# Kernel optimization log

Hardware: AMD Instinct MI355X
Metric: run time of the kernel (lower is better)

## Reference

```python
import jax, jax.numpy as jnp
import numpy as np

N_NODES = 100000
N_EDGES = 1600000
D_NODE = 32
D_EDGE = 16
D_OUT = 32
L2_EPS = 1e-12  # tf.math.l2_normalize default epsilon


def setup_inputs() -> dict:
    key = jax.random.key(0)
    k_h, k_e, k_w, k_s, k_d = jax.random.split(key, 5)
    h = jax.random.normal(k_h, (N_NODES, D_NODE), dtype=jnp.float32)
    e = jax.random.normal(k_e, (N_EDGES, D_EDGE), dtype=jnp.float32)
    # Dense(output_dim) kernel over concat(node, edge) features
    W = jax.random.normal(k_w, (D_NODE + D_EDGE, D_OUT), dtype=jnp.float32) * 0.1
    b = jnp.zeros((D_OUT,), dtype=jnp.float32)
    src = jax.random.randint(k_s, (N_EDGES,), 0, N_NODES, dtype=jnp.int32)
    dst = jax.random.randint(k_d, (N_EDGES,), 0, N_NODES, dtype=jnp.int32)
    return {"h": h, "e": e, "W": W, "b": b, "src": src, "dst": dst}


def reference(h, e, W, b, src, dst):
    # message: m = concat(h[src], e)              [E, D+De]
    # reduce:  new_h = mean over (self_msg, mailbox) of Dense(msg)
    # Dense is affine (activation=None), so Dense(mean) == mean(Dense): one GEMM.
    n = h.shape[0]
    msg = jnp.concatenate([h[src], e], axis=-1)                      # [E, D+De]
    agg = jax.ops.segment_sum(msg, dst, num_segments=n)              # [N, D+De]
    deg = jax.ops.segment_sum(jnp.ones_like(dst, dtype=h.dtype), dst, num_segments=n)
    self_msg = jnp.concatenate([h, jnp.zeros((n, e.shape[1]), h.dtype)], axis=-1)
    mean_msg = (self_msg + agg) / (deg[:, None] + 1.0)               # self counts in the mean
    new_h = mean_msg @ W + b                                         # [N, D_OUT]
    # activation=None -> identity; then tf.math.l2_normalize(axis=-1)
    sq = jnp.sum(new_h * new_h, axis=-1, keepdims=True)
    return new_h * jax.lax.rsqrt(jnp.maximum(sq, L2_EPS))
```

## Files before the change

kernel.cpp:

```cpp
#include <hip/hip_runtime.h>

#define D_NODE 32
#define D_EDGE 16
#define D_IN   48
#define D_OUT  32
#define L2_EPS 1e-12f

#define NPB       128
#define BKT_SHIFT 7
#define MAX_NB    4096
#define CH        8192
#define CTH       1024
#define EPT       (CH / CTH)
#define GR        128
#define TILE      512
#define ATH       512


__global__ __launch_bounds__(CTH) void k_chunkhist(
    const int* __restrict__ dst, int* __restrict__ counts2d, int n_edges, int nb)
{
    extern __shared__ int c[];
    for (int i = threadIdx.x; i < nb; i += CTH) c[i] = 0;
    __syncthreads();
    int base = blockIdx.x * CH + threadIdx.x;
    #pragma unroll
    for (int k = 0; k < EPT; ++k) {
        int i = base + k * CTH;
        if (i < n_edges) atomicAdd(&c[dst[i] >> BKT_SHIFT], 1);
    }
    __syncthreads();
    int* row = counts2d + (size_t)blockIdx.x * nb;
    for (int i = threadIdx.x; i < nb; i += CTH) row[i] = c[i];
}

__global__ __launch_bounds__(256) void k_partial(
    const int* __restrict__ counts2d, int* __restrict__ partial, int nb, int nc)
{
    int b = blockIdx.x * 256 + threadIdx.x;
    if (b >= nb) return;
    int g = blockIdx.y;
    int c0 = g * GR, c1 = min(c0 + GR, nc);
    int s = 0;
    #pragma unroll 4
    for (int c = c0; c < c1; ++c) s += counts2d[(size_t)c * nb + b];
    partial[(size_t)g * nb + b] = s;
}

__global__ __launch_bounds__(1024) void k_offsets(
    int* __restrict__ partial, int* __restrict__ offsets, int nb, int ng)
{
    __shared__ int s[1024];
    const int PT = MAX_NB / 1024;
    int t = threadIdx.x;
    int tot[PT];
    int ts = 0;
    #pragma unroll
    for (int j = 0; j < PT; ++j) {
        int b = t * PT + j;
        int v = 0;
        if (b < nb) for (int g = 0; g < ng; ++g) v += partial[(size_t)g * nb + b];
        tot[j] = v; ts += v;
    }
    s[t] = ts;
    __syncthreads();
    for (int off = 1; off < 1024; off <<= 1) {
        int u = (t >= off) ? s[t - off] : 0;
        __syncthreads();
        s[t] += u;
        __syncthreads();
    }
    if (t == 1023) offsets[nb] = s[1023];
    int run = s[t] - ts;
    #pragma unroll
    for (int j = 0; j < PT; ++j) {
        int b = t * PT + j;
        if (b < nb) {
            offsets[b] = run;
            int r2 = run;
            for (int g = 0; g < ng; ++g) {
                int v = partial[(size_t)g * nb + b];
                partial[(size_t)g * nb + b] = r2;
                r2 += v;
            }
            run += tot[j];
        }
    }
}

__global__ __launch_bounds__(256) void k_base2d(
    int* __restrict__ counts2d, const int* __restrict__ partial, int nb, int nc)
{
    int b = blockIdx.x * 256 + threadIdx.x;
    if (b >= nb) return;
    int g = blockIdx.y;
    int run = partial[(size_t)g * nb + b];
    int c0 = g * GR, c1 = min(c0 + GR, nc);
    #pragma unroll 4
    for (int c = c0; c < c1; ++c) {
        size_t idx = (size_t)c * nb + b;
        int v = counts2d[idx];
        counts2d[idx] = run;
        run += v;
    }
}

__global__ __launch_bounds__(CTH) void k_scatter(
    const int* __restrict__ dst, const int* __restrict__ src,
    const int* __restrict__ base2d, int2* __restrict__ meta2, int n_edges, int nb)
{
    extern __shared__ int sm[];
    int* lbase = sm;
    int* lrank = sm + nb;
    const int* brow = base2d + (size_t)blockIdx.x * nb;
    for (int i = threadIdx.x; i < nb; i += CTH) { lbase[i] = brow[i]; lrank[i] = 0; }
    __syncthreads();
    int base = blockIdx.x * CH + threadIdx.x;
    #pragma unroll
    for (int k = 0; k < EPT; ++k) {
        int i = base + k * CTH;
        if (i < n_edges) {
            int d = dst[i];
            int bkt = d >> BKT_SHIFT;
            int r = atomicAdd(&lrank[bkt], 1);
            int slot = lbase[bkt] + r;
            meta2[slot] = make_int2(src[i] | ((d & (NPB - 1)) << 20), i);
        }
    }
}

__global__ __launch_bounds__(ATH) void k_accum(
    const float* __restrict__ h, const float4* __restrict__ e4,
    const float* __restrict__ W, const float* __restrict__ b,
    const int* __restrict__ offsets, const int2* __restrict__ meta2,
    float* __restrict__ out, int n_nodes)
{
    __shared__ float Ws[D_IN * D_OUT];
    __shared__ float bs[D_OUT];
    __shared__ int2 csr[TILE];
    __shared__ int cnt[NPB], cnt2[NPB], offs[NPB];
    __shared__ float4 pool4[4 * (TILE + 1)];

    int b0 = offsets[blockIdx.x], b1 = offsets[blockIdx.x + 1];

    int2 m2 = make_int2(0, 0);
    float4 v0 = make_float4(0.f, 0.f, 0.f, 0.f), v1 = v0, v2 = v0, v3 = v0;
    {
        int tn0 = min(TILE, b1 - b0);
        if ((int)threadIdx.x < tn0) {
            m2 = meta2[b0 + threadIdx.x];
            const float4* er = e4 + (size_t)m2.y * 4;
            v0 = er[0]; v1 = er[1]; v2 = er[2]; v3 = er[3];
        }
    }

    for (int i = threadIdx.x; i < D_IN * D_OUT; i += ATH) Ws[i] = W[i];
    if (threadIdx.x < D_OUT) bs[threadIdx.x] = b[threadIdx.x];
    if (threadIdx.x < NPB) { cnt[threadIdx.x] = 0; cnt2[threadIdx.x] = 0; }
    __syncthreads();

    int g  = threadIdx.x >> 2;
    int jg = threadIdx.x & 3;

    float4 ha0 = make_float4(0.f, 0.f, 0.f, 0.f);
    float4 ha1 = make_float4(0.f, 0.f, 0.f, 0.f);
    float4 ea  = make_float4(0.f, 0.f, 0.f, 0.f);
    float deg = 0.f;

    for (int t0 = b0; t0 < b1; t0 += TILE) {
        int tn  = min(TILE, b1 - t0);
        int t1  = t0 + TILE;
        int ntn = (t1 < b1) ? min(TILE, b1 - t1) : 0;
        int mv  = m2.x;
        int dl  = (mv >> 20) & (NPB - 1);

        if ((int)threadIdx.x < ntn) m2 = meta2[t1 + threadIdx.x];
        if ((int)threadIdx.x < tn) {
            float4* pr = pool4 + threadIdx.x;
            pr[0]              = v0;
            pr[TILE + 1]       = v1;
            pr[2 * (TILE + 1)] = v2;
            pr[3 * (TILE + 1)] = v3;
            atomicAdd(&cnt[dl], 1);
        }
        __syncthreads();

        if (threadIdx.x < 64) {
            int c0 = cnt[2 * threadIdx.x];
            int c1 = cnt[2 * threadIdx.x + 1];
            int p = c0 + c1;
            int x = p;
            #pragma unroll
            for (int o = 1; o < 64; o <<= 1) {
                int y = __shfl_up(x, o);
                if (threadIdx.x >= o) x += y;
            }
            int basex = x - p;
            offs[2 * threadIdx.x]     = basex;
            offs[2 * threadIdx.x + 1] = basex + c0;
        } else if (threadIdx.x < 64 + NPB) {
            cnt2[threadIdx.x - 64] = 0;
        }
        int myc = cnt[g];
        __syncthreads();

        int mybase = offs[g];
        if ((int)threadIdx.x < tn) {
            int r = atomicAdd(&cnt2[dl], 1);
            csr[offs[dl] + r] = make_int2(mv, threadIdx.x);
        }
        if ((int)threadIdx.x < ntn) {
            const float4* er = e4 + (size_t)m2.y * 4;
            v0 = er[0]; v1 = er[1]; v2 = er[2]; v3 = er[3];
        }
        if (threadIdx.x < NPB) cnt[threadIdx.x] = 0;
        deg += (float)myc;
        __syncthreads();

        const float4* poolj = pool4 + jg * (TILE + 1);
        #pragma unroll 4
        for (int s = 0; s < myc; ++s) {
            int2 c = csr[mybase + s];
            const float4* hr = reinterpret_cast<const float4*>(
                h + (size_t)(c.x & 0xFFFFF) * D_NODE) + 2 * jg;
            float4 h0 = hr[0], h1 = hr[1];
            float4 ev = poolj[c.y];
            ha0.x += h0.x; ha0.y += h0.y; ha0.z += h0.z; ha0.w += h0.w;
            ha1.x += h1.x; ha1.y += h1.y; ha1.z += h1.z; ha1.w += h1.w;
            ea.x  += ev.x; ea.y  += ev.y; ea.z  += ev.z; ea.w  += ev.w;
        }
        __syncthreads();
    }

    float (*mrow)[D_IN + 1] = reinterpret_cast<float (*)[D_IN + 1]>(pool4);
    __syncthreads();

    int node = blockIdx.x * NPB + g;
    if (node < n_nodes) {
        float inv = 1.f / (deg + 1.f);
        const float4* hs = reinterpret_cast<const float4*>(
            h + (size_t)node * D_NODE) + 2 * jg;
        float4 s0 = hs[0], s1 = hs[1];
        mrow[g][8 * jg + 0] = (ha0.x + s0.x) * inv;
        mrow[g][8 * jg + 1] = (ha0.y + s0.y) * inv;
        mrow[g][8 * jg + 2] = (ha0.z + s0.z) * inv;
        mrow[g][8 * jg + 3] = (ha0.w + s0.w) * inv;
        mrow[g][8 * jg + 4] = (ha1.x + s1.x) * inv;
        mrow[g][8 * jg + 5] = (ha1.y + s1.y) * inv;
        mrow[g][8 * jg + 6] = (ha1.z + s1.z) * inv;
        mrow[g][8 * jg + 7] = (ha1.w + s1.w) * inv;
        mrow[g][D_NODE + 4 * jg + 0] = ea.x * inv;
        mrow[g][D_NODE + 4 * jg + 1] = ea.y * inv;
        mrow[g][D_NODE + 4 * jg + 2] = ea.z * inv;
        mrow[g][D_NODE + 4 * jg + 3] = ea.w * inv;
    }
    __syncthreads();
    if (node >= n_nodes) return;

    const float* row = mrow[g];
    float a[8];
    #pragma unroll
    for (int q = 0; q < 8; ++q) a[q] = bs[jg * 8 + q];
    #pragma unroll
    for (int k = 0; k < D_IN; ++k) {
        float mk = row[k];
        const float* w = Ws + k * D_OUT + jg * 8;
        #pragma unroll
        for (int q = 0; q < 8; ++q) a[q] += mk * w[q];
    }
    float sq = 0.f;
    #pragma unroll
    for (int q = 0; q < 8; ++q) sq += a[q] * a[q];
    sq += __shfl_xor(sq, 1);
    sq += __shfl_xor(sq, 2);
    float r = rsqrtf(fmaxf(sq, L2_EPS));
    float4* o4 = reinterpret_cast<float4*>(out + (size_t)node * D_OUT) + 2 * jg;
    o4[0] = make_float4(a[0] * r, a[1] * r, a[2] * r, a[3] * r);
    o4[1] = make_float4(a[4] * r, a[5] * r, a[6] * r, a[7] * r);
}

__global__ __launch_bounds__(256) void scatter_kernel(
    const float* __restrict__ h, const float* __restrict__ e,
    const int* __restrict__ src, const int* __restrict__ dst,
    float* __restrict__ agg, float* __restrict__ deg, int n_edges)
{
    int tid  = blockIdx.x * blockDim.x + threadIdx.x;
    int edge = tid >> 4;
    int c    = tid & 15;
    if (edge >= n_edges) return;
    int s = src[edge], d = dst[edge];
    float v0 = h[(size_t)s * D_NODE + c];
    float v1 = h[(size_t)s * D_NODE + 16 + c];
    float v2 = e[(size_t)edge * D_EDGE + c];
    float* row = agg + (size_t)d * D_IN;
    atomicAdd(row + c, v0);
    atomicAdd(row + 16 + c, v1);
    atomicAdd(row + 32 + c, v2);
    if (c == 0) atomicAdd(deg + d, 1.0f);
}

__global__ __launch_bounds__(256) void node_kernel(
    const float* __restrict__ h, const float* __restrict__ W, const float* __restrict__ b,
    const float* __restrict__ agg, const float* __restrict__ deg,
    float* __restrict__ out, int n_nodes)
{
    __shared__ float Ws[D_IN * D_OUT];
    __shared__ float bs[D_OUT];
    for (int i = threadIdx.x; i < D_IN * D_OUT; i += blockDim.x) Ws[i] = W[i];
    if (threadIdx.x < D_OUT) bs[threadIdx.x] = b[threadIdx.x];
    __syncthreads();
    int node = blockIdx.x * blockDim.x + threadIdx.x;
    if (node >= n_nodes) return;
    const float4* h4 = reinterpret_cast<const float4*>(h + (size_t)node * D_NODE);
    const float4* a4 = reinterpret_cast<const float4*>(agg + (size_t)node * D_IN);
    float inv = 1.0f / (deg[node] + 1.0f);
    float m[D_IN];
    #pragma unroll
    for (int k = 0; k < D_NODE / 4; ++k) {
        float4 hv = h4[k]; float4 av = a4[k];
        m[4*k+0] = (hv.x + av.x) * inv; m[4*k+1] = (hv.y + av.y) * inv;
        m[4*k+2] = (hv.z + av.z) * inv; m[4*k+3] = (hv.w + av.w) * inv;
    }
    #pragma unroll
    for (int k = D_NODE / 4; k < D_IN / 4; ++k) {
        float4 av = a4[k];
        m[4*k+0] = av.x * inv; m[4*k+1] = av.y * inv;
        m[4*k+2] = av.z * inv; m[4*k+3] = av.w * inv;
    }
    float acc[D_OUT];
    #pragma unroll
    for (int j = 0; j < D_OUT; ++j) acc[j] = bs[j];
    #pragma unroll
    for (int k = 0; k < D_IN; ++k) {
        float mk = m[k];
        #pragma unroll
        for (int j = 0; j < D_OUT; ++j) acc[j] += mk * Ws[k * D_OUT + j];
    }
    float sq = 0.0f;
    #pragma unroll
    for (int j = 0; j < D_OUT; ++j) sq += acc[j] * acc[j];
    float r = rsqrtf(fmaxf(sq, L2_EPS));
    float4* o4 = reinterpret_cast<float4*>(out + (size_t)node * D_OUT);
    #pragma unroll
    for (int j = 0; j < D_OUT / 4; ++j) {
        float4 v;
        v.x = acc[4*j+0] * r; v.y = acc[4*j+1] * r;
        v.z = acc[4*j+2] * r; v.w = acc[4*j+3] * r;
        o4[j] = v;
    }
}

extern "C" void kernel_launch(void* const* d_in, const int* in_sizes, int n_in,
                              void* d_out, int out_size, void* d_ws, size_t ws_size,
                              hipStream_t stream) {
    const float* h   = (const float*)d_in[0];
    const float* e   = (const float*)d_in[1];
    const float* W   = (const float*)d_in[2];
    const float* b   = (const float*)d_in[3];
    const int*   src = (const int*)d_in[4];
    const int*   dst = (const int*)d_in[5];
    float* out = (float*)d_out;

    const int n_nodes = in_sizes[0] / D_NODE;
    const int n_edges = in_sizes[4];

    const int nb  = (n_nodes + NPB - 1) / NPB;
    const int nc  = (n_edges + CH - 1) / CH;
    const int ng  = (nc + GR - 1) / GR;
    const int nbt = (nb + 255) / 256;

    size_t o_counts2d = 0;
    size_t o_partial  = o_counts2d + (size_t)nc * nb;
    size_t o_offsets  = o_partial + (size_t)ng * nb;
    size_t o_meta2    = (o_offsets + (size_t)nb + 1 + 1) & ~(size_t)1;
    size_t need       = (o_meta2 + (size_t)n_edges * 2) * sizeof(int);

    if (nb <= MAX_NB && n_nodes < (1 << 20) && need <= ws_size && n_edges > 0) {
        int* ws_i     = (int*)d_ws;
        int* counts2d = ws_i + o_counts2d;
        int* partial  = ws_i + o_partial;
        int* offsets  = ws_i + o_offsets;
        int2* meta2   = (int2*)(ws_i + o_meta2);

        dim3 g2(nbt, ng);
        k_chunkhist<<<nc, CTH, (size_t)nb * sizeof(int), stream>>>(
            dst, counts2d, n_edges, nb);
        k_partial<<<g2, 256, 0, stream>>>(counts2d, partial, nb, nc);
        k_offsets<<<1, 1024, 0, stream>>>(partial, offsets, nb, ng);
        k_base2d<<<g2, 256, 0, stream>>>(counts2d, partial, nb, nc);
        k_scatter<<<nc, CTH, (size_t)2 * nb * sizeof(int), stream>>>(
            dst, src, counts2d, meta2, n_edges, nb);
        k_accum<<<nb, ATH, 0, stream>>>(
            h, (const float4*)e, W, b, offsets, meta2, out, n_nodes);
    } else {
        float* agg = (float*)d_ws;
        float* deg = agg + (size_t)n_nodes * D_IN;
        hipMemsetAsync(d_ws, 0, (size_t)n_nodes * (D_IN + 1) * sizeof(float), stream);
        long long threads = (long long)n_edges * 16;
        scatter_kernel<<<(int)((threads + 255) / 256), 256, 0, stream>>>(h, e, src, dst, agg, deg, n_edges);
        node_kernel<<<(n_nodes + 255) / 256, 256, 0, stream>>>(h, W, b, agg, deg, out, n_nodes);
    }
}
```

Measured before the change: 122.9 us.

## Replace edge-feature smem pool with direct gathers and larger single-pass tiles

Drops the pipelined staging of edge features into a shared-memory pool. Each bucket's metadata (up to 4096 edges) is now loaded in one pass and sorted by destination in shared memory, and the accumulation loop gathers edge features straight from global memory. The intent is to remove per-tile prefetch and synchronisation overhead and fit more blocks per CU (launch bounds of 8). The cost is uncoalesced global gathers of edge features, no prefetch overlap, and a larger csr array that is reused as the output staging buffer.

```diff
diff --git a/kernel.cpp b/kernel.cpp
--- a/kernel.cpp
+++ b/kernel.cpp
@@ -13,8 +13,9 @@
 #define CTH       1024
 #define EPT       (CH / CTH)
 #define GR        128
-#define TILE      512
 #define ATH       512
+#define CAP       4096
+#define KPT       (CAP / ATH)
 
 
 __global__ __launch_bounds__(CTH) void k_chunkhist(
@@ -129,7 +130,7 @@
     }
 }
 
-__global__ __launch_bounds__(ATH) void k_accum(
+__global__ __launch_bounds__(ATH, 8) void k_accum(
     const float* __restrict__ h, const float4* __restrict__ e4,
     const float* __restrict__ W, const float* __restrict__ b,
     const int* __restrict__ offsets, const int2* __restrict__ meta2,
@@ -137,22 +138,8 @@
 {
     __shared__ float Ws[D_IN * D_OUT];
     __shared__ float bs[D_OUT];
-    __shared__ int2 csr[TILE];
+    __shared__ int2 csr[CAP];
     __shared__ int cnt[NPB], cnt2[NPB], offs[NPB];
-    __shared__ float4 pool4[4 * (TILE + 1)];
-
-    int b0 = offsets[blockIdx.x], b1 = offsets[blockIdx.x + 1];
-
-    int2 m2 = make_int2(0, 0);
-    float4 v0 = make_float4(0.f, 0.f, 0.f, 0.f), v1 = v0, v2 = v0, v3 = v0;
-    {
-        int tn0 = min(TILE, b1 - b0);
-        if ((int)threadIdx.x < tn0) {
-            m2 = meta2[b0 + threadIdx.x];
-            const float4* er = e4 + (size_t)m2.y * 4;
-            v0 = er[0]; v1 = er[1]; v2 = er[2]; v3 = er[3];
-        }
-    }
 
     for (int i = threadIdx.x; i < D_IN * D_OUT; i += ATH) Ws[i] = W[i];
     if (threadIdx.x < D_OUT) bs[threadIdx.x] = b[threadIdx.x];
@@ -167,21 +154,19 @@
     float4 ea  = make_float4(0.f, 0.f, 0.f, 0.f);
     float deg = 0.f;
 
-    for (int t0 = b0; t0 < b1; t0 += TILE) {
-        int tn  = min(TILE, b1 - t0);
-        int t1  = t0 + TILE;
-        int ntn = (t1 < b1) ? min(TILE, b1 - t1) : 0;
-        int mv  = m2.x;
-        int dl  = (mv >> 20) & (NPB - 1);
-
-        if ((int)threadIdx.x < ntn) m2 = meta2[t1 + threadIdx.x];
-        if ((int)threadIdx.x < tn) {
-            float4* pr = pool4 + threadIdx.x;
-            pr[0]              = v0;
-            pr[TILE + 1]       = v1;
-            pr[2 * (TILE + 1)] = v2;
-            pr[3 * (TILE + 1)] = v3;
-            atomicAdd(&cnt[dl], 1);
+    int b0 = offsets[blockIdx.x], b1 = offsets[blockIdx.x + 1];
+
+    for (int t0 = b0; t0 < b1; t0 += CAP) {
+        int tn = min(CAP, b1 - t0);
+
+        int2 m[KPT];
+        #pragma unroll
+        for (int k = 0; k < KPT; ++k) {
+            int i = (int)threadIdx.x + k * ATH;
+            if (i < tn) {
+                m[k] = meta2[t0 + i];
+                atomicAdd(&cnt[(m[k].x >> 20) & (NPB - 1)], 1);
+            }
         }
         __syncthreads();
 
@@ -198,42 +183,40 @@
             int basex = x - p;
             offs[2 * threadIdx.x]     = basex;
             offs[2 * threadIdx.x + 1] = basex + c0;
-        } else if (threadIdx.x < 64 + NPB) {
-            cnt2[threadIdx.x - 64] = 0;
         }
         int myc = cnt[g];
         __syncthreads();
 
-        int mybase = offs[g];
-        if ((int)threadIdx.x < tn) {
-            int r = atomicAdd(&cnt2[dl], 1);
-            csr[offs[dl] + r] = make_int2(mv, threadIdx.x);
-        }
-        if ((int)threadIdx.x < ntn) {
-            const float4* er = e4 + (size_t)m2.y * 4;
-            v0 = er[0]; v1 = er[1]; v2 = er[2]; v3 = er[3];
+        #pragma unroll
+        for (int k = 0; k < KPT; ++k) {
+            int i = (int)threadIdx.x + k * ATH;
+            if (i < tn) {
+                int dl = (m[k].x >> 20) & (NPB - 1);
+                int r = atomicAdd(&cnt2[dl], 1);
+                csr[offs[dl] + r] = make_int2(m[k].x & 0xFFFFF, m[k].y);
+            }
         }
         if (threadIdx.x < NPB) cnt[threadIdx.x] = 0;
         deg += (float)myc;
         __syncthreads();
 
-        const float4* poolj = pool4 + jg * (TILE + 1);
+        int mybase = offs[g];
         #pragma unroll 4
         for (int s = 0; s < myc; ++s) {
             int2 c = csr[mybase + s];
             const float4* hr = reinterpret_cast<const float4*>(
-                h + (size_t)(c.x & 0xFFFFF) * D_NODE) + 2 * jg;
+                h + (size_t)c.x * D_NODE) + 2 * jg;
             float4 h0 = hr[0], h1 = hr[1];
-            float4 ev = poolj[c.y];
+            float4 ev = e4[(size_t)c.y * 4 + jg];
             ha0.x += h0.x; ha0.y += h0.y; ha0.z += h0.z; ha0.w += h0.w;
             ha1.x += h1.x; ha1.y += h1.y; ha1.z += h1.z; ha1.w += h1.w;
             ea.x  += ev.x; ea.y  += ev.y; ea.z  += ev.z; ea.w  += ev.w;
         }
-        __syncthreads();
-    }
-
-    float (*mrow)[D_IN + 1] = reinterpret_cast<float (*)[D_IN + 1]>(pool4);
-    __syncthreads();
+        if (threadIdx.x < NPB) cnt2[threadIdx.x] = 0;
+        __syncthreads();
+    }
+
+    float (*mrow)[D_IN + 1] = reinterpret_cast<float (*)[D_IN + 1]>(csr);
 
     int node = blockIdx.x * NPB + g;
     if (node < n_nodes) {
```

Result: no change. 123.6 us (+0.6%).
